# Performance work log

Hardware: AMD Instinct MI355X
Metric: run time of the kernel (lower is better)

## Reference

```python
import jax, jax.numpy as jnp
import numpy as np

B, IN, OUT, TDIM, YDIM = 4096, 48, 64, 128, 64
HID = OUT * OUT  # 4096, Y_layer hidden/output width


def setup_inputs() -> dict:
    key = jax.random.key(0)
    ks = jax.random.split(key, 9)
    x = jax.random.normal(ks[0], (B, IN, IN), dtype=jnp.float32)
    # symmetrize so input is SPD-like (module assumes SPD inputs)
    x = 0.5 * (x + jnp.swapaxes(x, 1, 2))
    t = jax.random.normal(ks[1], (B, TDIM), dtype=jnp.float32)
    Y = jax.random.normal(ks[2], (B, YDIM), dtype=jnp.float32)
    # Stiefel (orthogonal) weight [input_size(=OUT after increase), output_size]
    W, _ = jnp.linalg.qr(jax.random.normal(ks[3], (OUT, OUT), dtype=jnp.float32))
    # Y_layer MLP params: Linear(YDIM,HID) -> SiLU -> Linear(HID,HID)
    Y_W1 = jax.random.normal(ks[4], (YDIM, HID), dtype=jnp.float32) / np.sqrt(YDIM)
    Y_b1 = jnp.zeros((HID,), dtype=jnp.float32)
    Y_W2 = jax.random.normal(ks[5], (HID, HID), dtype=jnp.float32) / np.sqrt(HID)
    Y_b2 = jnp.zeros((HID,), dtype=jnp.float32)
    return {"input": x, "t": t, "Y": Y, "W": W,
            "Y_W1": Y_W1, "Y_b1": Y_b1, "Y_W2": Y_W2, "Y_b2": Y_b2}


def reference(input, t, Y, W, Y_W1, Y_b1, Y_W2, Y_b2):
    # Y_layer MLP -> per-sample transform emb_Y [B, OUT, OUT]
    h = jax.nn.silu(Y @ Y_W1 + Y_b1)
    emb_Y = (h @ Y_W2 + Y_b2).reshape(B, OUT, OUT)
    # SPDIncreaseDim: embed input in top-left of OUTxOUT, ones on padded diagonal
    pad = OUT - IN
    xp = jnp.pad(input, ((0, 0), (0, pad), (0, pad)))
    add_diag = jnp.concatenate([jnp.zeros(IN, input.dtype), jnp.ones(pad, input.dtype)])
    xp = xp + jnp.diag(add_diag)[None]
    # congruence with Stiefel weight: W^T X W
    out = jnp.einsum('ji,bjk,kl->bil', W, xp, W)
    # congruence with MLP-generated weight: emb_Y X emb_Y^T
    out = jnp.einsum('bij,bjk,blk->bil', emb_Y, out, emb_Y)
    return out
```

## Files before the change

kernel.cpp:

```cpp
#include <hip/hip_runtime.h>
#include <hip/hip_bf16.h>

typedef __bf16 bf16;
typedef __bf16 bf16x8 __attribute__((ext_vector_type(8)));
typedef float floatx4 __attribute__((ext_vector_type(4)));

#define MFMA16(a, b, c) __builtin_amdgcn_mfma_f32_16x16x32_bf16((a), (b), (c), 0, 0, 0)

__device__ inline void gload_lds16(const void* g, void* l) {
    __builtin_amdgcn_global_load_lds((__attribute__((address_space(1))) void*)g,
                                     (__attribute__((address_space(3))) void*)l, 16, 0, 0);
}

__global__ __launch_bounds__(256) void prep_fused(
    const float* __restrict__ W2,
    const float* __restrict__ W,
    const float* __restrict__ b2,
    const float* __restrict__ Y,
    const float* __restrict__ W1,
    const float* __restrict__ b1,
    bf16* __restrict__ W2fT,
    float* __restrict__ b2f,
    bf16* __restrict__ h)
{
    __shared__ __align__(16) char smem[45056];
    int t = threadIdx.x, bid = blockIdx.x;
    int w = t >> 6, l = t & 63;
    int lm = l & 15, q2 = l >> 4, q8 = q2 * 8;

    if (bid < 2048) {
        int pt = bid & 31, i = bid >> 5;
        bf16* sW = (bf16*)smem;
        bf16* sA = sW + 64 * 72;
        bf16* sT = sA + 128 * 72;
        int p0 = pt * 128;

#pragma unroll
        for (int kk = 0; kk < 16; kk++) {
            int idx = t + 256 * kk;
            sW[(idx >> 6) * 72 + (idx & 63)] = (bf16)W[idx];
        }
        {
            const float* src = W2 + (size_t)p0 * 4096 + i * 64;
#pragma unroll
            for (int kk = 0; kk < 8; kk++) {
                int c = t + 256 * kk;
                int row = c >> 4, j4 = (c & 15) * 4;
                float4 v = *(const float4*)(src + (size_t)row * 4096 + j4);
                bf16 tmp[4] = {(bf16)v.x, (bf16)v.y, (bf16)v.z, (bf16)v.w};
                *(uint2*)(sA + row * 72 + j4) = *(const uint2*)tmp;
            }
        }
        __syncthreads();

        floatx4 acc[2][4] = {};
#pragma unroll
        for (int kc = 0; kc < 2; kc++) {
            bf16x8 a0 = *(const bf16x8*)(sA + (w * 32 + lm) * 72 + kc * 32 + q8);
            bf16x8 a1 = *(const bf16x8*)(sA + (w * 32 + 16 + lm) * 72 + kc * 32 + q8);
#pragma unroll
            for (int jn = 0; jn < 4; jn++) {
                bf16x8 bf_ = *(const bf16x8*)(sW + (jn * 16 + lm) * 72 + kc * 32 + q8);
                acc[0][jn] = MFMA16(a0, bf_, acc[0][jn]);
                acc[1][jn] = MFMA16(a1, bf_, acc[1][jn]);
            }
        }
#pragma unroll
        for (int im = 0; im < 2; im++)
#pragma unroll
            for (int jn = 0; jn < 4; jn++) {
                int pr = w * 32 + im * 16 + q2 * 4;
                int lc = jn * 16 + lm;
                union { bf16 h4[4]; uint2 u; } pk;
#pragma unroll
                for (int r = 0; r < 4; r++) pk.h4[r] = (bf16)acc[im][jn][r];
                *(uint2*)(sT + lc * 136 + pr) = pk.u;
            }
        __syncthreads();
#pragma unroll
        for (int kk = 0; kk < 4; kk++) {
            int c = t + 256 * kk;
            int row = c >> 4, off = (c & 15) * 8;
            uint4 v = *(const uint4*)(sT + row * 136 + off);
            *(uint4*)(W2fT + (size_t)(i * 64 + row) * 4096 + p0 + off) = v;
        }
        return;
    }

    if (bid < 2112) {
        int i = bid - 2048;
        if (t < 64) {
            float acc = 0.f;
            const float* b2r = b2 + i * 64;
            const float* wr_ = W + t * 64;
#pragma unroll
            for (int j = 0; j < 64; j++) acc = fmaf(b2r[j], wr_[j], acc);
            b2f[i * 64 + t] = acc;
        }
        return;
    }

    {
        int q = bid - 2112;
        int m0 = (q >> 5) * 128, n0 = (q & 31) * 128;
        bf16* sY = (bf16*)smem;
        bf16* sWT = sY + 128 * 72;

#pragma unroll
        for (int kk = 0; kk < 8; kk++) {
            int c = t + 256 * kk;
            int row = c >> 4, c4 = (c & 15) * 4;
            float4 v = *(const float4*)(Y + (size_t)(m0 + row) * 64 + c4);
            bf16 tmp[4] = {(bf16)v.x, (bf16)v.y, (bf16)v.z, (bf16)v.w};
            *(uint2*)(sY + row * 72 + c4) = *(const uint2*)tmp;
        }
#pragma unroll
        for (int kk = 0; kk < 8; kk++) {
            int c = t + 256 * kk;
            int k = c >> 5, j4 = (c & 31) * 4;
            float4 v = *(const float4*)(W1 + (size_t)k * 4096 + n0 + j4);
            sWT[(j4 + 0) * 72 + k] = (bf16)v.x;
            sWT[(j4 + 1) * 72 + k] = (bf16)v.y;
            sWT[(j4 + 2) * 72 + k] = (bf16)v.z;
            sWT[(j4 + 3) * 72 + k] = (bf16)v.w;
        }
        __syncthreads();

        int wn = (w & 1) * 64, wm = (w >> 1) * 64;
        floatx4 acc[4][4] = {};
#pragma unroll
        for (int kc = 0; kc < 2; kc++) {
            bf16x8 af[4], bfr[4];
#pragma unroll
            for (int i = 0; i < 4; i++)
                af[i] = *(const bf16x8*)(sWT + (wn + i * 16 + lm) * 72 + kc * 32 + q8);
#pragma unroll
            for (int j = 0; j < 4; j++)
                bfr[j] = *(const bf16x8*)(sY + (wm + j * 16 + lm) * 72 + kc * 32 + q8);
#pragma unroll
            for (int i = 0; i < 4; i++)
#pragma unroll
                for (int j = 0; j < 4; j++)
                    acc[i][j] = MFMA16(af[i], bfr[j], acc[i][j]);
        }
#pragma unroll
        for (int i = 0; i < 4; i++) {
            int nb = n0 + wn + i * 16 + q2 * 4;
            float4 bv = *(const float4*)(b1 + nb);
            float bb[4] = {bv.x, bv.y, bv.z, bv.w};
#pragma unroll
            for (int j = 0; j < 4; j++) {
                int m = m0 + wm + j * 16 + lm;
                union { bf16 h4[4]; uint2 u; } pk;
#pragma unroll
                for (int r = 0; r < 4; r++) {
                    float v = acc[i][j][r] + bb[r];
                    v = v / (1.f + __expf(-v));
                    pk.h4[r] = (bf16)v;
                }
                *(uint2*)(h + (size_t)m * 4096 + nb) = pk.u;
            }
        }
    }
}

__global__ __launch_bounds__(512, 2) void gemm_bt_bias(
    const bf16* __restrict__ A, const bf16* __restrict__ BT,
    const float* __restrict__ bias, bf16* __restrict__ C,
    int M, int N, int K)
{
    __shared__ __align__(16) char lds[131072];

    int t = threadIdx.x, w = t >> 6, l = t & 63;
    int lm = l & 15, q2 = l >> 4;
    int wm = w >> 2, wn = w & 3;

    int bid = blockIdx.x;
    int wg = (bid & 7) * 32 + (bid >> 3);
    int m0 = (wg >> 4) * 256, n0 = (wg & 15) * 256;

    int c1 = t + 512;
    int ks0 = ((t & 3) ^ ((t >> 3) & 3)) * 8;
    int ks1 = ((c1 & 3) ^ ((c1 >> 3) & 3)) * 8;
    const bf16* gA0 = A + (size_t)(m0 + (t >> 2)) * K + ks0;
    const bf16* gA1 = A + (size_t)(m0 + (c1 >> 2)) * K + ks1;
    const bf16* gB0 = BT + (size_t)(n0 + (t >> 2)) * K + ks0;
    const bf16* gB1 = BT + (size_t)(n0 + (c1 >> 2)) * K + ks1;
    const int dst0 = (w * 64) * 16, dst1 = (512 + w * 64) * 16;

    auto issue = [&](int slot) {
        char* slab = lds + slot * 32768;
        gload_lds16(gA0, slab + dst0);
        gload_lds16(gA1, slab + dst1);
        gload_lds16(gB0, slab + 16384 + dst0);
        gload_lds16(gB1, slab + 16384 + dst1);
        gA0 += 32; gA1 += 32; gB0 += 32; gB1 += 32;
    };

    const int qp16 = (q2 ^ ((lm >> 1) & 3)) * 16;
    const int aoff = (wm * 128 + lm) * 64 + qp16;
    const int boff = 16384 + (wn * 64 + lm) * 64 + qp16;

    floatx4 acc[8][4] = {};

    auto body = [&](int kt, bool doIssue) {
        __builtin_amdgcn_s_barrier();
        __builtin_amdgcn_sched_barrier(0);
        asm volatile("" ::: "memory");
        if (doIssue) issue((kt + 3) & 3);
        const char* slab = lds + (kt & 3) * 32768;
        bf16x8 av[8], bv[4];
#pragma unroll
        for (int j = 0; j < 4; j++) bv[j] = *(const bf16x8*)(slab + boff + j * 1024);
#pragma unroll
        for (int i = 0; i < 4; i++) av[i] = *(const bf16x8*)(slab + aoff + i * 1024);
        __builtin_amdgcn_s_setprio(1);
#pragma unroll
        for (int i = 0; i < 4; i++)
#pragma unroll
            for (int j = 0; j < 4; j++) acc[i][j] = MFMA16(av[i], bv[j], acc[i][j]);
#pragma unroll
        for (int i = 4; i < 8; i++) av[i] = *(const bf16x8*)(slab + aoff + i * 1024);
#pragma unroll
        for (int i = 4; i < 8; i++)
#pragma unroll
            for (int j = 0; j < 4; j++) acc[i][j] = MFMA16(av[i], bv[j], acc[i][j]);
        __builtin_amdgcn_s_setprio(0);
    };

    issue(0); issue(1); issue(2);
    const int KT = K >> 5;
    for (int kt = 0; kt < KT - 2; ++kt) {
        asm volatile("s_waitcnt vmcnt(8)" ::: "memory");
        body(kt, kt < KT - 3);
    }
    asm volatile("s_waitcnt vmcnt(4)" ::: "memory");
    body(KT - 2, false);
    asm volatile("s_waitcnt vmcnt(0)" ::: "memory");
    body(KT - 1, false);

#pragma unroll
    for (int i = 0; i < 8; i++) {
        int r0 = m0 + wm * 128 + i * 16 + q2 * 4;
#pragma unroll
        for (int j = 0; j < 4; j++) {
            int cc = n0 + wn * 64 + j * 16 + lm;
            float bb = bias[cc];
#pragma unroll
            for (int r = 0; r < 4; r++)
                C[(size_t)(r0 + r) * N + cc] = (bf16)(acc[i][j][r] + bb);
        }
    }
}

#define ST 72
__global__ __launch_bounds__(256) void batched_congruence(
    const float* __restrict__ x,
    const bf16* __restrict__ F,
    float* __restrict__ out)
{
    __shared__ bf16 sX[64 * ST], sF[64 * ST], sT[64 * ST];
    int t = threadIdx.x, w = t >> 6, l = t & 63;
    int b = blockIdx.x;
    int lm = l & 15, q2 = l >> 4, q8 = q2 * 8;
    int r0 = (w >> 1) * 32, c0 = (w & 1) * 32;

    const float4* xb = (const float4*)(x + (size_t)b * 2304);
    float4 v0 = xb[t];
    float4 v1 = xb[t + 256];
    float4 v2 = (t < 64) ? xb[t + 512] : make_float4(0.f, 0.f, 0.f, 0.f);

    {
        const uint4* gf = (const uint4*)(F + (size_t)b * 4096);
#pragma unroll
        for (int kk = 0; kk < 2; kk++) {
            int c = t + 256 * kk;
            *(uint4*)(sF + (c >> 3) * ST + (c & 7) * 8) = gf[c];
        }
    }
    {
        unsigned* sx32 = (unsigned*)sX;
#pragma unroll
        for (int kk = 0; kk < 4; kk++) {
            int idx = t + 256 * kk;
            if (idx < 384) {
                int r = idx >> 3, d = 24 + (idx & 7);
                sx32[r * 36 + d] = 0u;
            } else if (idx < 896) {
                int k2 = idx - 384;
                int r = 48 + (k2 >> 5), d = k2 & 31;
                unsigned val = 0u;
                if (d == (r >> 1)) val = (r & 1) ? 0x3F800000u : 0x00003F80u;
                sx32[r * 36 + d] = val;
            }
        }
    }
    {
        int c = t;
        bf16 p4[4];
        p4[0] = (bf16)v0.x; p4[1] = (bf16)v0.y; p4[2] = (bf16)v0.z; p4[3] = (bf16)v0.w;
        *(uint2*)(sX + (c / 12) * ST + (c % 12) * 4) = *(const uint2*)p4;
        c = t + 256;
        p4[0] = (bf16)v1.x; p4[1] = (bf16)v1.y; p4[2] = (bf16)v1.z; p4[3] = (bf16)v1.w;
        *(uint2*)(sX + (c / 12) * ST + (c % 12) * 4) = *(const uint2*)p4;
        if (t < 64) {
            c = t + 512;
            p4[0] = (bf16)v2.x; p4[1] = (bf16)v2.y; p4[2] = (bf16)v2.z; p4[3] = (bf16)v2.w;
            *(uint2*)(sX + (c / 12) * ST + (c % 12) * 4) = *(const uint2*)p4;
        }
    }
    __syncthreads();

    auto mm = [&](const bf16* PA, const bf16* PB, floatx4 acc[2][2]) {
#pragma unroll
        for (int kc = 0; kc < 2; kc++) {
            bf16x8 a0 = *(const bf16x8*)(PA + (r0 + lm) * ST + kc * 32 + q8);
            bf16x8 a1 = *(const bf16x8*)(PA + (r0 + 16 + lm) * ST + kc * 32 + q8);
            bf16x8 b0 = *(const bf16x8*)(PB + (c0 + lm) * ST + kc * 32 + q8);
            bf16x8 b1 = *(const bf16x8*)(PB + (c0 + 16 + lm) * ST + kc * 32 + q8);
            acc[0][0] = MFMA16(a0, b0, acc[0][0]);
            acc[0][1] = MFMA16(a0, b1, acc[0][1]);
            acc[1][0] = MFMA16(a1, b0, acc[1][0]);
            acc[1][1] = MFMA16(a1, b1, acc[1][1]);
        }
    };

    floatx4 z = {0.f, 0.f, 0.f, 0.f};
    {
        floatx4 acc[2][2] = {{z, z}, {z, z}};
        mm(sX, sF, acc);
#pragma unroll
        for (int i = 0; i < 2; i++)
#pragma unroll
            for (int j = 0; j < 2; j++) {
                int R = r0 + i * 16 + q2 * 4;
                int Cc = c0 + j * 16 + lm;
                union { bf16 h4[4]; uint2 u; } pk;
#pragma unroll
                for (int r = 0; r < 4; r++) pk.h4[r] = (bf16)acc[i][j][r];
                *(uint2*)(sT + Cc * ST + R) = pk.u;
            }
    }
    __syncthreads();
    {
        floatx4 acc[2][2] = {{z, z}, {z, z}};
        mm(sT, sF, acc);
#pragma unroll
        for (int i = 0; i < 2; i++)
#pragma unroll
            for (int j = 0; j < 2; j++) {
                int R = r0 + i * 16 + q2 * 4;
                int Cc = c0 + j * 16 + lm;
#pragma unroll
                for (int r = 0; r < 4; r++)
                    out[(size_t)b * 4096 + (size_t)(R + r) * 64 + Cc] = acc[i][j][r];
            }
    }
}

extern "C" void kernel_launch(void* const* d_in, const int* in_sizes, int n_in,
                              void* d_out, int out_size, void* d_ws, size_t ws_size,
                              hipStream_t stream) {
    const float* x  = (const float*)d_in[0];
    const float* Y  = (const float*)d_in[2];
    const float* W  = (const float*)d_in[3];
    const float* W1 = (const float*)d_in[4];
    const float* b1 = (const float*)d_in[5];
    const float* W2 = (const float*)d_in[6];
    const float* b2 = (const float*)d_in[7];
    float* out = (float*)d_out;

    const size_t NN = (size_t)4096 * 4096;
    bf16* h    = (bf16*)d_ws;
    bf16* W2fT = h + NN;
    bf16* emb  = W2fT + NN;
    float* b2f = (float*)d_out;

    prep_fused<<<3136, 256, 0, stream>>>(W2, W, b2, Y, W1, b1, W2fT, b2f, h);
    gemm_bt_bias<<<256, 512, 0, stream>>>(h, W2fT, b2f, emb, 4096, 4096, 4096);
    batched_congruence<<<4096, 256, 0, stream>>>(x, emb, out);
}
```

Baseline: 303.1 us.

## Split GEMM k-step into two phases with interleaved A/B prefetch and vectorized stores

Each k-iteration of the big bf16 GEMM becomes two barrier-separated phases. A's next-tile global-to-LDS loads are issued in the first phase and B's in the second, each after that phase's LDS reads, with explicit lgkmcnt waits and sched barriers pinning the order. The MFMA operands are swapped so each lane holds four consecutive output columns, which lets the epilogue read bias as a float4 and store four bf16 values in one 8-byte write. The aim is finer overlap of memory traffic with MFMA and fewer scalar stores, at the cost of an extra barrier per k-step.

```diff
diff --git a/kernel.cpp b/kernel.cpp
--- a/kernel.cpp
+++ b/kernel.cpp
@@ -188,13 +188,17 @@
     const bf16* gB1 = BT + (size_t)(n0 + (c1 >> 2)) * K + ks1;
     const int dst0 = (w * 64) * 16, dst1 = (512 + w * 64) * 16;
 
-    auto issue = [&](int slot) {
+    auto issueA = [&](int slot) {
         char* slab = lds + slot * 32768;
         gload_lds16(gA0, slab + dst0);
         gload_lds16(gA1, slab + dst1);
+        gA0 += 32; gA1 += 32;
+    };
+    auto issueB = [&](int slot) {
+        char* slab = lds + slot * 32768;
         gload_lds16(gB0, slab + 16384 + dst0);
         gload_lds16(gB1, slab + 16384 + dst1);
-        gA0 += 32; gA1 += 32; gB0 += 32; gB1 += 32;
+        gB0 += 32; gB1 += 32;
     };
 
     const int qp16 = (q2 ^ ((lm >> 1) & 3)) * 16;
@@ -204,51 +208,68 @@
     floatx4 acc[8][4] = {};
 
     auto body = [&](int kt, bool doIssue) {
+        const char* slab = lds + (kt & 3) * 32768;
+        int s = (kt + 3) & 3;
         __builtin_amdgcn_s_barrier();
         __builtin_amdgcn_sched_barrier(0);
         asm volatile("" ::: "memory");
-        if (doIssue) issue((kt + 3) & 3);
-        const char* slab = lds + (kt & 3) * 32768;
-        bf16x8 av[8], bv[4];
+        bf16x8 bv[4], a0[4], a1[4];
 #pragma unroll
         for (int j = 0; j < 4; j++) bv[j] = *(const bf16x8*)(slab + boff + j * 1024);
 #pragma unroll
-        for (int i = 0; i < 4; i++) av[i] = *(const bf16x8*)(slab + aoff + i * 1024);
+        for (int i = 0; i < 4; i++) a0[i] = *(const bf16x8*)(slab + aoff + i * 1024);
+        if (doIssue) issueA(s);
+        asm volatile("s_waitcnt lgkmcnt(0)" ::: "memory");
+        __builtin_amdgcn_sched_barrier(0);
         __builtin_amdgcn_s_setprio(1);
 #pragma unroll
         for (int i = 0; i < 4; i++)
 #pragma unroll
-            for (int j = 0; j < 4; j++) acc[i][j] = MFMA16(av[i], bv[j], acc[i][j]);
-#pragma unroll
-        for (int i = 4; i < 8; i++) av[i] = *(const bf16x8*)(slab + aoff + i * 1024);
-#pragma unroll
-        for (int i = 4; i < 8; i++)
-#pragma unroll
-            for (int j = 0; j < 4; j++) acc[i][j] = MFMA16(av[i], bv[j], acc[i][j]);
+            for (int j = 0; j < 4; j++) acc[i][j] = MFMA16(bv[j], a0[i], acc[i][j]);
         __builtin_amdgcn_s_setprio(0);
+        __builtin_amdgcn_sched_barrier(0);
+        __builtin_amdgcn_s_barrier();
+        __builtin_amdgcn_sched_barrier(0);
+#pragma unroll
+        for (int i = 0; i < 4; i++) a1[i] = *(const bf16x8*)(slab + aoff + (4 + i) * 1024);
+        if (doIssue) issueB(s);
+        asm volatile("s_waitcnt lgkmcnt(0)" ::: "memory");
+        __builtin_amdgcn_sched_barrier(0);
+        __builtin_amdgcn_s_setprio(1);
+#pragma unroll
+        for (int i = 0; i < 4; i++)
+#pragma unroll
+            for (int j = 0; j < 4; j++) acc[4 + i][j] = MFMA16(bv[j], a1[i], acc[4 + i][j]);
+        __builtin_amdgcn_s_setprio(0);
+        __builtin_amdgcn_sched_barrier(0);
     };
 
-    issue(0); issue(1); issue(2);
+    issueA(0); issueB(0); issueA(1); issueB(1); issueA(2); issueB(2);
     const int KT = K >> 5;
     for (int kt = 0; kt < KT - 2; ++kt) {
         asm volatile("s_waitcnt vmcnt(8)" ::: "memory");
+        __builtin_amdgcn_sched_barrier(0);
         body(kt, kt < KT - 3);
     }
     asm volatile("s_waitcnt vmcnt(4)" ::: "memory");
+    __builtin_amdgcn_sched_barrier(0);
     body(KT - 2, false);
     asm volatile("s_waitcnt vmcnt(0)" ::: "memory");
+    __builtin_amdgcn_sched_barrier(0);
     body(KT - 1, false);
 
 #pragma unroll
     for (int i = 0; i < 8; i++) {
-        int r0 = m0 + wm * 128 + i * 16 + q2 * 4;
+        int m = m0 + wm * 128 + i * 16 + lm;
 #pragma unroll
         for (int j = 0; j < 4; j++) {
-            int cc = n0 + wn * 64 + j * 16 + lm;
-            float bb = bias[cc];
-#pragma unroll
-            for (int r = 0; r < 4; r++)
-                C[(size_t)(r0 + r) * N + cc] = (bf16)(acc[i][j][r] + bb);
+            int nb = n0 + wn * 64 + j * 16 + q2 * 4;
+            float4 b4 = *(const float4*)(bias + nb);
+            float bb[4] = {b4.x, b4.y, b4.z, b4.w};
+            union { bf16 h4[4]; uint2 u; } pk;
+#pragma unroll
+            for (int r = 0; r < 4; r++) pk.h4[r] = (bf16)(acc[i][j][r] + bb[r]);
+            *(uint2*)(C + (size_t)m * N + nb) = pk.u;
         }
     }
 }
```

Measured after the change: 307.0 us. No clear change (+1.3%).

## Restructure GEMM to 4 waves with 128x128 warp tiles and double-buffered register fragments

Applied to the files above, without the earlier changes.

The 4096^3 bf16 GEMM now runs 256 threads per block, and each wave computes a 128x128 tile (64 MFMAs per k-step) instead of 128x64. LDS fragments are double-buffered in registers: the next k-step's reads and global-to-LDS issues happen while the current MFMAs run, gated by explicit lgkmcnt/vmcnt waits. The MFMA operands are swapped so the output can be written as packed 4-wide bf16 stores with vectorized bias loads. The aim is a higher MFMA-to-LDS-read ratio and better latency hiding, at the cost of much higher register pressure (256 accumulator floats per lane) and fewer waves to hide latency.

```diff
diff --git a/kernel.cpp b/kernel.cpp
--- a/kernel.cpp
+++ b/kernel.cpp
@@ -164,7 +164,7 @@
     }
 }
 
-__global__ __launch_bounds__(512, 2) void gemm_bt_bias(
+__global__ __launch_bounds__(256, 1) void gemm_bt_bias(
     const bf16* __restrict__ A, const bf16* __restrict__ BT,
     const float* __restrict__ bias, bf16* __restrict__ C,
     int M, int N, int K)
@@ -173,84 +173,124 @@
 
     int t = threadIdx.x, w = t >> 6, l = t & 63;
     int lm = l & 15, q2 = l >> 4;
-    int wm = w >> 2, wn = w & 3;
+    int wm = w >> 1, wn = w & 1;
 
     int bid = blockIdx.x;
     int wg = (bid & 7) * 32 + (bid >> 3);
     int m0 = (wg >> 4) * 256, n0 = (wg & 15) * 256;
 
-    int c1 = t + 512;
-    int ks0 = ((t & 3) ^ ((t >> 3) & 3)) * 8;
-    int ks1 = ((c1 & 3) ^ ((c1 >> 3) & 3)) * 8;
-    const bf16* gA0 = A + (size_t)(m0 + (t >> 2)) * K + ks0;
-    const bf16* gA1 = A + (size_t)(m0 + (c1 >> 2)) * K + ks1;
-    const bf16* gB0 = BT + (size_t)(n0 + (t >> 2)) * K + ks0;
-    const bf16* gB1 = BT + (size_t)(n0 + (c1 >> 2)) * K + ks1;
-    const int dst0 = (w * 64) * 16, dst1 = (512 + w * 64) * 16;
+    const bf16 *gA[4], *gB[4];
+#pragma unroll
+    for (int kk = 0; kk < 4; kk++) {
+        int c = t + 256 * kk;
+        int row = c >> 2;
+        int ph = ((c & 3) ^ ((c >> 3) & 3)) * 8;
+        gA[kk] = A + (size_t)(m0 + row) * K + ph;
+        gB[kk] = BT + (size_t)(n0 + row) * K + ph;
+    }
+    const int wbase = w * 1024;
 
     auto issue = [&](int slot) {
-        char* slab = lds + slot * 32768;
-        gload_lds16(gA0, slab + dst0);
-        gload_lds16(gA1, slab + dst1);
-        gload_lds16(gB0, slab + 16384 + dst0);
-        gload_lds16(gB1, slab + 16384 + dst1);
-        gA0 += 32; gA1 += 32; gB0 += 32; gB1 += 32;
+        char* slab = lds + (slot << 15);
+#pragma unroll
+        for (int kk = 0; kk < 4; kk++) {
+            gload_lds16(gA[kk], slab + kk * 4096 + wbase);
+            gA[kk] += 32;
+        }
+#pragma unroll
+        for (int kk = 0; kk < 4; kk++) {
+            gload_lds16(gB[kk], slab + 16384 + kk * 4096 + wbase);
+            gB[kk] += 32;
+        }
     };
 
     const int qp16 = (q2 ^ ((lm >> 1) & 3)) * 16;
     const int aoff = (wm * 128 + lm) * 64 + qp16;
-    const int boff = 16384 + (wn * 64 + lm) * 64 + qp16;
-
-    floatx4 acc[8][4] = {};
-
-    auto body = [&](int kt, bool doIssue) {
-        __builtin_amdgcn_s_barrier();
-        __builtin_amdgcn_sched_barrier(0);
-        asm volatile("" ::: "memory");
-        if (doIssue) issue((kt + 3) & 3);
-        const char* slab = lds + (kt & 3) * 32768;
-        bf16x8 av[8], bv[4];
-#pragma unroll
-        for (int j = 0; j < 4; j++) bv[j] = *(const bf16x8*)(slab + boff + j * 1024);
-#pragma unroll
-        for (int i = 0; i < 4; i++) av[i] = *(const bf16x8*)(slab + aoff + i * 1024);
+    const int boff = 16384 + (wn * 128 + lm) * 64 + qp16;
+
+    floatx4 acc[8][8] = {};
+    bf16x8 fa0[8], fb0[8], fa1[8], fb1[8];
+
+    auto readF = [&](bf16x8* fa, bf16x8* fb, int slot) {
+        const char* slab = lds + (slot << 15);
+#pragma unroll
+        for (int j = 0; j < 8; j++) fb[j] = *(const bf16x8*)(slab + boff + j * 1024);
+#pragma unroll
+        for (int i = 0; i < 8; i++) fa[i] = *(const bf16x8*)(slab + aoff + i * 1024);
+    };
+    auto mfma64 = [&](const bf16x8* fa, const bf16x8* fb) {
         __builtin_amdgcn_s_setprio(1);
 #pragma unroll
-        for (int i = 0; i < 4; i++)
-#pragma unroll
-            for (int j = 0; j < 4; j++) acc[i][j] = MFMA16(av[i], bv[j], acc[i][j]);
-#pragma unroll
-        for (int i = 4; i < 8; i++) av[i] = *(const bf16x8*)(slab + aoff + i * 1024);
-#pragma unroll
-        for (int i = 4; i < 8; i++)
-#pragma unroll
-            for (int j = 0; j < 4; j++) acc[i][j] = MFMA16(av[i], bv[j], acc[i][j]);
+        for (int i = 0; i < 8; i++)
+#pragma unroll
+            for (int j = 0; j < 8; j++) acc[i][j] = MFMA16(fb[j], fa[i], acc[i][j]);
         __builtin_amdgcn_s_setprio(0);
     };
 
+#define GATE15 do { __builtin_amdgcn_sched_barrier(0); \
+    asm volatile("s_waitcnt lgkmcnt(15)" ::: "memory"); \
+    __builtin_amdgcn_sched_barrier(0); } while (0)
+#define BOT(vm) do { asm volatile("s_waitcnt vmcnt(" #vm ")" ::: "memory"); \
+    __builtin_amdgcn_s_barrier(); \
+    __builtin_amdgcn_sched_barrier(0); } while (0)
+
     issue(0); issue(1); issue(2);
+    asm volatile("s_waitcnt vmcnt(8)" ::: "memory");
+    __builtin_amdgcn_s_barrier();
+    __builtin_amdgcn_sched_barrier(0);
+    readF(fa0, fb0, 0);
+
     const int KT = K >> 5;
-    for (int kt = 0; kt < KT - 2; ++kt) {
-        asm volatile("s_waitcnt vmcnt(8)" ::: "memory");
-        body(kt, kt < KT - 3);
-    }
-    asm volatile("s_waitcnt vmcnt(4)" ::: "memory");
-    body(KT - 2, false);
-    asm volatile("s_waitcnt vmcnt(0)" ::: "memory");
-    body(KT - 1, false);
-
+    for (int kt = 0; kt < KT - 4; kt += 2) {
+        readF(fa1, fb1, (kt + 1) & 3);
+        issue((kt + 3) & 3);
+        GATE15;
+        mfma64(fa0, fb0);
+        BOT(8);
+        readF(fa0, fb0, (kt + 2) & 3);
+        issue((kt + 4) & 3);
+        GATE15;
+        mfma64(fa1, fb1);
+        BOT(8);
+    }
+    readF(fa1, fb1, (KT - 3) & 3);
+    issue((KT - 1) & 3);
+    GATE15;
+    mfma64(fa0, fb0);
+    BOT(8);
+    readF(fa0, fb0, (KT - 2) & 3);
+    GATE15;
+    mfma64(fa1, fb1);
+    BOT(0);
+    readF(fa1, fb1, (KT - 1) & 3);
+    GATE15;
+    mfma64(fa0, fb0);
+    asm volatile("s_waitcnt lgkmcnt(0)" ::: "memory");
+    __builtin_amdgcn_sched_barrier(0);
+    mfma64(fa1, fb1);
+
+#undef GATE15
+#undef BOT
+
+    float4 bb[8];
+#pragma unroll
+    for (int j = 0; j < 8; j++)
+        bb[j] = *(const float4*)(bias + n0 + wn * 128 + j * 16 + q2 * 4);
 #pragma unroll
     for (int i = 0; i < 8; i++) {
-        int r0 = m0 + wm * 128 + i * 16 + q2 * 4;
-#pragma unroll
-        for (int j = 0; j < 4; j++) {
-            int cc = n0 + wn * 64 + j * 16 + lm;
-            float bb = bias[cc];
-#pragma unroll
-            for (int r = 0; r < 4; r++)
-                C[(size_t)(r0 + r) * N + cc] = (bf16)(acc[i][j][r] + bb);
-        }
-    }
+        int m = m0 + wm * 128 + i * 16 + lm;
+#pragma unroll
+        for (int j = 0; j < 8; j++) {
+            int nb = n0 + wn * 128 + j * 16 + q2 * 4;
+            union { bf16 h4[4]; uint2 u; } pk;
+            pk.h4[0] = (bf16)(acc[i][j][0] + bb[j].x);
+            pk.h4[1] = (bf16)(acc[i][j][1] + bb[j].y);
+            pk.h4[2] = (bf16)(acc[i][j][2] + bb[j].z);
+            pk.h4[3] = (bf16)(acc[i][j][3] + bb[j].w);
+            *(uint2*)(C + (size_t)m * N + nb) = pk.u;
+        }
+    }
+    (void)M;
 }
 
 #define ST 72
@@ -377,6 +417,6 @@
     float* b2f = (float*)d_out;
 
     prep_fused<<<3136, 256, 0, stream>>>(W2, W, b2, Y, W1, b1, W2fT, b2f, h);
-    gemm_bt_bias<<<256, 512, 0, stream>>>(h, W2fT, b2f, emb, 4096, 4096, 4096);
+    gemm_bt_bias<<<256, 256, 0, stream>>>(h, W2fT, b2f, emb, 4096, 4096, 4096);
     batched_congruence<<<4096, 256, 0, stream>>>(x, emb, out);
 }
```

New measurement: 321.0 us. 1.06x slower.
